# Kernel tuning notes

Hardware: AMD Instinct MI355X
Metric: run time of the kernel (lower is better)

Reference implementation:

```python
import jax, jax.numpy as jnp
import numpy as np

B, S, D, H = 4, 4096, 256, 4
Dh = D // H


def setup_inputs() -> dict:
    key = jax.random.key(0)
    ks = jax.random.split(key, 5)
    scale = 1.0 / np.sqrt(D)
    return {
        "inputs": jax.random.normal(ks[0], (B, S, D), dtype=jnp.float32),
        "Wq": jax.random.normal(ks[1], (D, D), dtype=jnp.float32) * scale,
        "bq": jnp.zeros((D,), jnp.float32),
        "Wk": jax.random.normal(ks[2], (D, D), dtype=jnp.float32) * scale,
        "bk": jnp.zeros((D,), jnp.float32),
        "Wv": jax.random.normal(ks[3], (D, D), dtype=jnp.float32) * scale,
        "bv": jnp.zeros((D,), jnp.float32),
        "Wo": jax.random.normal(ks[4], (D, D), dtype=jnp.float32) * scale,
        "bo": jnp.zeros((D,), jnp.float32),
    }


def reference(inputs, Wq, bq, Wk, bk, Wv, bv, Wo, bo):
    b, s, d = inputs.shape
    # QKV projections
    q = inputs @ Wq + bq
    k = inputs @ Wk + bk
    v = inputs @ Wv + bv
    # separate heads: [B, S, D] -> [B, H, S, Dh]
    def split_heads(x):
        return x.reshape(b, s, H, Dh).transpose(0, 2, 1, 3)
    q, k, v = split_heads(q), split_heads(k), split_heads(v)
    # scaled dot-product attention (no causal mask: mask=False)
    scores = jnp.einsum("bhqd,bhkd->bhqk", q, k) / jnp.sqrt(jnp.float32(Dh))
    weights = jax.nn.softmax(scores, axis=-1)
    attn = jnp.einsum("bhqk,bhkd->bhqd", weights, v)
    # combine heads: [B, H, S, Dh] -> [B, S, D]
    attn = attn.transpose(0, 2, 1, 3).reshape(b, s, d)
    return attn @ Wo + bo
```

## Files before the change

### kernel.cpp

```cpp
#include <hip/hip_runtime.h>
#include <cmath>

#define B_  4
#define S_  4096
#define D_  256
#define H_  4
#define DH_ 64
#define M_TOTAL (B_*S_)
#define QSCALE 0.1803368801111f

typedef __bf16 bf16x8 __attribute__((ext_vector_type(8)));
typedef __bf16 bf16x4 __attribute__((ext_vector_type(4)));
typedef __bf16 bf16x2 __attribute__((ext_vector_type(2)));
typedef float  f32x4  __attribute__((ext_vector_type(4)));
typedef float  f32x16 __attribute__((ext_vector_type(16)));

#define AS1 __attribute__((address_space(1)))
#define AS3 __attribute__((address_space(3)))

__device__ __forceinline__ void g2lds16(const void* g, void* l) {
    __builtin_amdgcn_global_load_lds((AS1 const void*)g, (AS3 void*)l, 16, 0, 0);
}

#if __has_builtin(__builtin_amdgcn_permlane32_swap)
typedef unsigned uint2v __attribute__((ext_vector_type(2)));
__device__ __forceinline__ void plswap(unsigned &a, unsigned &b) {
    uint2v r = __builtin_amdgcn_permlane32_swap(a, b, false, false);
    a = r[0]; b = r[1];
}
#else
__device__ __forceinline__ void plswap(unsigned &a, unsigned &b) {
    unsigned bl = (unsigned)__shfl_xor((int)b, 32);
    unsigned ah = (unsigned)__shfl_xor((int)a, 32);
    bool hi = (threadIdx.x & 32) != 0;
    unsigned na = hi ? bl : a;
    unsigned nb = hi ? b  : ah;
    a = na; b = nb;
}
#endif

__device__ __forceinline__ unsigned pk2(float x, float y) {
    bf16x2 t; t[0] = (__bf16)x; t[1] = (__bf16)y;
    return __builtin_bit_cast(unsigned, t);
}

__global__ __launch_bounds__(256) void prep(const float* __restrict__ X,
                                            const float* __restrict__ W0,
                                            const float* __restrict__ W1,
                                            const float* __restrict__ W2,
                                            const float* __restrict__ W3,
                                            __bf16* __restrict__ Xb,
                                            __bf16* __restrict__ Wt_all) {
    int t = threadIdx.x;
    if (blockIdx.x < 2048) {
        size_t i = ((size_t)blockIdx.x * 256 + t) * 8;
        float4 v0 = *(const float4*)(X + i);
        float4 v1 = *(const float4*)(X + i + 4);
        bf16x8 o;
        o[0] = (__bf16)v0.x; o[1] = (__bf16)v0.y; o[2] = (__bf16)v0.z; o[3] = (__bf16)v0.w;
        o[4] = (__bf16)v1.x; o[5] = (__bf16)v1.y; o[6] = (__bf16)v1.z; o[7] = (__bf16)v1.w;
        *(bf16x8*)(Xb + i) = o;
        return;
    }
    int bid = blockIdx.x - 2048;
    int z = bid >> 6, rem = bid & 63;
    int by = rem >> 3, bx = rem & 7;
    const float* W = (z == 0) ? W0 : (z == 1) ? W1 : (z == 2) ? W2 : W3;
    float wsc = (z == 0) ? QSCALE : 1.0f;
    __bf16* Wt = Wt_all + (size_t)z * 65536;
    __shared__ float tile[32][33];
    int r0 = by * 32, c0 = bx * 32;
#pragma unroll
    for (int e = 0; e < 4; e++) {
        int idx = t + e * 256; int r = idx >> 5, c = idx & 31;
        tile[r][c] = W[(r0 + r) * 256 + c0 + c];
    }
    __syncthreads();
#pragma unroll
    for (int e = 0; e < 4; e++) {
        int idx = t + e * 256; int r = idx >> 5, c = idx & 31;
        Wt[(c0 + r) * 256 + (r0 + c)] = (__bf16)(tile[c][r] * wsc);
    }
}

__global__ __launch_bounds__(256) void gemm_bt(const __bf16* __restrict__ A,
                                               const __bf16* __restrict__ Wt_all,
                                               const float* __restrict__ bias0,
                                               const float* __restrict__ bias1,
                                               const float* __restrict__ bias2,
                                               __bf16* __restrict__ outb,
                                               __bf16* __restrict__ voutb,
                                               float* __restrict__ outf,
                                               int out_is_f32, float bsc0) {
    constexpr int K = 256;
    __shared__ __attribute__((aligned(16))) __bf16 As[128 * 32];
    __shared__ __attribute__((aligned(16))) __bf16 Bs[128 * 32];

    int t = threadIdx.x;
    int lane = t & 63, w = t >> 6;
    int wr = w >> 1, wc = w & 1;
    int l16 = lane & 15, quad = lane >> 4;
    int mbase = blockIdx.x * 128;
    int nbase = blockIdx.y * 128;
    int z = blockIdx.z;
    const __bf16* Bt = Wt_all + (size_t)z * 65536;
    const float* bias = (z == 0) ? bias0 : (z == 1) ? bias1 : bias2;
    float bscale = (z == 0) ? bsc0 : 1.0f;

    f32x4 acc[4][4] = {};

    int srow = t >> 2;
    int sseg = (t & 3) * 8;

    for (int kk = 0; kk < K; kk += 32) {
        __syncthreads();
        g2lds16(A  + (size_t)(mbase +      srow) * K + kk + sseg, (char*)As +        t * 16);
        g2lds16(A  + (size_t)(mbase + 64 + srow) * K + kk + sseg, (char*)As + 4096 + t * 16);
        g2lds16(Bt + (size_t)(nbase +      srow) * K + kk + sseg, (char*)Bs +        t * 16);
        g2lds16(Bt + (size_t)(nbase + 64 + srow) * K + kk + sseg, (char*)Bs + 4096 + t * 16);
        __syncthreads();

        bf16x8 a[4], b[4];
#pragma unroll
        for (int i = 0; i < 4; i++)
            a[i] = *(const bf16x8*)(As + (wr * 64 + i * 16 + l16) * 32 + quad * 8);
#pragma unroll
        for (int j = 0; j < 4; j++)
            b[j] = *(const bf16x8*)(Bs + (wc * 64 + j * 16 + l16) * 32 + quad * 8);
#pragma unroll
        for (int i = 0; i < 4; i++)
#pragma unroll
            for (int j = 0; j < 4; j++)
                acc[i][j] = __builtin_amdgcn_mfma_f32_16x16x32_bf16(a[i], b[j], acc[i][j], 0, 0, 0);
    }

#pragma unroll
    for (int i = 0; i < 4; i++) {
#pragma unroll
        for (int j = 0; j < 4; j++) {
            int col = nbase + wc * 64 + j * 16 + l16;
            float bv = bias[col] * bscale;
            int row0 = mbase + wr * 64 + i * 16 + quad * 4;
            if (out_is_f32) {
#pragma unroll
                for (int r = 0; r < 4; r++)
                    outf[(size_t)(row0 + r) * 256 + col] = acc[i][j][r] + bv;
            } else if (z == 2) {
                int hcol = col >> 6, dh = col & 63;
                int bidx = row0 >> 12, s0 = row0 & 4095;
                bf16x4 pk;
#pragma unroll
                for (int r = 0; r < 4; r++) pk[r] = (__bf16)(acc[i][j][r] + bv);
                *(bf16x4*)(voutb + ((size_t)(bidx * 4 + hcol) * 64 + dh) * 4096 + s0) = pk;
            } else {
#pragma unroll
                for (int r = 0; r < 4; r++)
                    outb[(size_t)z * ((size_t)M_TOTAL * 256) + (size_t)(row0 + r) * 256 + col] =
                        (__bf16)(acc[i][j][r] + bv);
            }
        }
    }
}

__global__ __launch_bounds__(256, 2) void attn(const __bf16* __restrict__ Qb,
                                               const __bf16* __restrict__ Kb,
                                               const __bf16* __restrict__ Vt,
                                               __bf16* __restrict__ Ctx) {
    __shared__ __attribute__((aligned(16))) __bf16 smem[32768];

    int t = threadIdx.x;
    int lane = t & 63, w = t >> 6;
    int l31 = lane & 31, hh = lane >> 5;
    int kw = w & 1, qw2 = w >> 1;

    int lin = blockIdx.x;
    int xcd = lin & 7, j = lin >> 3;
    int bh = xcd * 2 + (j & 1);
    int qblk = j >> 1;
    int b = bh >> 2, hd = bh & 3;
    int qw = qblk * 128 + qw2 * 64;

    const __bf16* Kbase = Kb + (size_t)b * S_ * 256 + hd * 64;
    const __bf16* Vbase = Vt + (size_t)bh * 64 * S_;

    bf16x8 qf[4][2];
#pragma unroll
    for (int ks = 0; ks < 4; ks++)
#pragma unroll
        for (int qt = 0; qt < 2; qt++)
            qf[ks][qt] = *(const bf16x8*)(Qb + (size_t)(b * S_ + qw + qt * 32 + l31) * 256
                                              + hd * 64 + ks * 16 + hh * 8);

    f32x16 acc[2][2] = {};
    float lsum[2] = {0.f, 0.f};

    int srow = t >> 3;
    int sseg = t & 7;

#define STAGE(kv, slot) do {                                                   \
        char* mk = (char*)smem + (slot) * 16384;                               \
        char* mv = mk + 8192;                                                  \
        _Pragma("unroll")                                                      \
        for (int c = 0; c < 2; c++) {                                          \
            int rr = c * 32 + srow;                                            \
            int gseg = (sseg ^ (rr & 7)) * 8;                                  \
            g2lds16(Kbase + (size_t)((kv) + rr) * 256 + gseg,                  \
                    mk + c * 4096 + t * 16);                                   \
            g2lds16(Vbase + (size_t)rr * S_ + (kv) + gseg,                     \
                    mv + c * 4096 + t * 16);                                   \
        }                                                                      \
    } while (0)

    STAGE(0, 0);
    STAGE(64, 1);

    for (int it = 0; it < 64; it++) {
        if (it < 62) {
            STAGE((it + 2) * 64, (it + 2) & 3);
            asm volatile("s_waitcnt vmcnt(8)" ::: "memory");
        } else if (it == 62) {
            asm volatile("s_waitcnt vmcnt(4)" ::: "memory");
        } else {
            asm volatile("s_waitcnt vmcnt(0)" ::: "memory");
        }
        asm volatile("s_barrier" ::: "memory");

        __bf16* Ksp = (__bf16*)((char*)smem + (it & 3) * 16384);
        __bf16* Vsp = Ksp + 4096;

        bf16x8 kf[4];
#pragma unroll
        for (int ks = 0; ks < 4; ks++) {
            int slot = (ks * 2 + hh) ^ (l31 & 7);
            kf[ks] = *(const bf16x8*)(Ksp + (kw * 32 + l31) * 64 + slot * 8);
        }
        f32x16 st[2] = {};
#pragma unroll
        for (int ks = 0; ks < 4; ks++)
#pragma unroll
            for (int qt = 0; qt < 2; qt++)
                st[qt] = __builtin_amdgcn_mfma_f32_32x32x16_bf16(kf[ks], qf[ks][qt], st[qt], 0, 0, 0);

        unsigned dd[2][8];
#pragma unroll
        for (int qt = 0; qt < 2; qt++) {
            float p[16];
#pragma unroll
            for (int r = 0; r < 16; r++) p[r] = __builtin_amdgcn_exp2f(st[qt][r]);
            float s0 = ((p[0] + p[1]) + (p[2] + p[3])) + ((p[4] + p[5]) + (p[6] + p[7]));
            float s1 = ((p[8] + p[9]) + (p[10] + p[11])) + ((p[12] + p[13]) + (p[14] + p[15]));
            lsum[qt] += s0 + s1;
#pragma unroll
            for (int m = 0; m < 4; m++) {
                dd[qt][m * 2]     = pk2(p[4 * m],     p[4 * m + 1]);
                dd[qt][m * 2 + 1] = pk2(p[4 * m + 2], p[4 * m + 3]);
            }
        }

#pragma unroll
        for (int tt = 0; tt < 2; tt++) {
            int tks = kw * 2 + tt;
            bf16x8 pf[2];
#pragma unroll
            for (int qt = 0; qt < 2; qt++) {
                unsigned x0 = dd[qt][4 * tt],     y0 = dd[qt][4 * tt + 2];
                unsigned x1 = dd[qt][4 * tt + 1], y1 = dd[qt][4 * tt + 3];
                plswap(x0, y0);
                plswap(x1, y1);
                union { unsigned u[4]; bf16x8 v; } c;
                c.u[0] = x0; c.u[1] = x1; c.u[2] = y0; c.u[3] = y1;
                pf[qt] = c.v;
            }
#pragma unroll
            for (int mt = 0; mt < 2; mt++) {
                int slot = (tks * 2 + hh) ^ (l31 & 7);
                bf16x8 vf = *(const bf16x8*)(Vsp + (mt * 32 + l31) * 64 + slot * 8);
#pragma unroll
                for (int qt = 0; qt < 2; qt++)
                    acc[mt][qt] = __builtin_amdgcn_mfma_f32_32x32x16_bf16(vf, pf[qt], acc[mt][qt], 0, 0, 0);
            }
        }
    }
#undef STAGE

#pragma unroll
    for (int qt = 0; qt < 2; qt++)
        lsum[qt] += __shfl_xor(lsum[qt], 32);

    __syncthreads();
    float* lsd = (float*)((char*)smem + 32768);
    if (kw == 1) {
#pragma unroll
        for (int mt = 0; mt < 2; mt++)
#pragma unroll
            for (int qt = 0; qt < 2; qt++)
#pragma unroll
                for (int g = 0; g < 4; g++) {
                    f32x4 v;
#pragma unroll
                    for (int e = 0; e < 4; e++) v[e] = acc[mt][qt][4 * g + e];
                    *(f32x4*)((char*)smem + qw2 * 16384
                              + ((mt * 2 + qt) * 4 + g) * 1024 + lane * 16) = v;
                }
        lsd[qw2 * 128 + lane * 2 + 0] = lsum[0];
        lsd[qw2 * 128 + lane * 2 + 1] = lsum[1];
    }
    __syncthreads();
    if (kw == 0) {
        float inv[2];
#pragma unroll
        for (int qt = 0; qt < 2; qt++)
            inv[qt] = 1.f / (lsum[qt] + lsd[qw2 * 128 + lane * 2 + qt]);
#pragma unroll
        for (int mt = 0; mt < 2; mt++)
#pragma unroll
            for (int qt = 0; qt < 2; qt++)
#pragma unroll
                for (int g = 0; g < 4; g++) {
                    f32x4 v = *(const f32x4*)((char*)smem + qw2 * 16384
                                              + ((mt * 2 + qt) * 4 + g) * 1024 + lane * 16);
#pragma unroll
                    for (int e = 0; e < 4; e++) acc[mt][qt][4 * g + e] += v[e];
                }

        __bf16* Es = smem + 18432 + qw2 * 4608;
#pragma unroll
        for (int qt = 0; qt < 2; qt++)
#pragma unroll
            for (int mt = 0; mt < 2; mt++)
#pragma unroll
                for (int rg = 0; rg < 4; rg++) {
                    bf16x4 ov;
#pragma unroll
                    for (int e = 0; e < 4; e++)
                        ov[e] = (__bf16)(acc[mt][qt][4 * rg + e] * inv[qt]);
                    int dhb = mt * 32 + rg * 8 + 4 * hh;
                    *(bf16x4*)(Es + (qt * 32 + l31) * 72 + dhb) = ov;
                }
#pragma unroll
        for (int pass = 0; pass < 8; pass++) {
            int q = pass * 8 + (lane >> 3);
            int col = (lane & 7) * 8;
            bf16x8 val = *(const bf16x8*)(Es + q * 72 + col);
            *(bf16x8*)(Ctx + (size_t)(b * S_ + qw + q) * 256 + hd * 64 + col) = val;
        }
    }
}

extern "C" void kernel_launch(void* const* d_in, const int* in_sizes, int n_in,
                              void* d_out, int out_size, void* d_ws, size_t ws_size,
                              hipStream_t stream) {
    const float* X  = (const float*)d_in[0];
    const float* Wq = (const float*)d_in[1];
    const float* bq = (const float*)d_in[2];
    const float* Wk = (const float*)d_in[3];
    const float* bk = (const float*)d_in[4];
    const float* Wv = (const float*)d_in[5];
    const float* bv = (const float*)d_in[6];
    const float* Wo = (const float*)d_in[7];
    const float* bo = (const float*)d_in[8];
    float* out = (float*)d_out;

    char* ws = (char*)d_ws;
    const size_t MB = 1024 * 1024;
    __bf16* Xb  = (__bf16*)(ws);
    __bf16* Ctx = (__bf16*)(ws);
    __bf16* Wt  = (__bf16*)(ws + 8 * MB);
    __bf16* Qb  = (__bf16*)(ws + 8 * MB + 512 * 1024);
    __bf16* Kb  = (__bf16*)((char*)Qb + 8 * MB);
    __bf16* Vt  = (__bf16*)((char*)Kb + 8 * MB);

    prep<<<dim3(2304), dim3(256), 0, stream>>>(X, Wq, Wk, Wv, Wo, Xb, Wt);
    gemm_bt<<<dim3(M_TOTAL / 128, 2, 3), dim3(256), 0, stream>>>(
        Xb, Wt, bq, bk, bv, Qb, Vt, nullptr, 0, QSCALE);
    attn<<<dim3(512), dim3(256), 0, stream>>>(Qb, Kb, Vt, Ctx);
    gemm_bt<<<dim3(M_TOTAL / 128, 2, 1), dim3(256), 0, stream>>>(
        Ctx, Wt + 3 * 65536, bo, bo, bo, nullptr, nullptr, out, 1, 1.0f);
}
```

Measured before the change: 178.3 us.

## Grow attention blocks to 1024 threads with 4-way KV split and 128-key tiles

The attention kernel now uses 1024-thread blocks covering 256 queries. Each query group is split across four KV-partition waves instead of two, and K/V are staged in 128-key tiles with double buffering in place of four 64-key slots. Each staged tile is shared by more waves and there are half as many loop iterations and barriers. The cost is a deeper sequential cross-wave reduction, with three extra barriers at the end, a wait for all outstanding loads before every iteration, and only 256 blocks, which may leave CUs underused.

```diff
diff --git a/kernel.cpp b/kernel.cpp
--- a/kernel.cpp
+++ b/kernel.cpp
@@ -162,23 +162,23 @@
     }
 }
 
-__global__ __launch_bounds__(256, 2) void attn(const __bf16* __restrict__ Qb,
-                                               const __bf16* __restrict__ Kb,
-                                               const __bf16* __restrict__ Vt,
-                                               __bf16* __restrict__ Ctx) {
+__global__ __launch_bounds__(1024, 4) void attn(const __bf16* __restrict__ Qb,
+                                                const __bf16* __restrict__ Kb,
+                                                const __bf16* __restrict__ Vt,
+                                                __bf16* __restrict__ Ctx) {
     __shared__ __attribute__((aligned(16))) __bf16 smem[32768];
 
     int t = threadIdx.x;
     int lane = t & 63, w = t >> 6;
     int l31 = lane & 31, hh = lane >> 5;
-    int kw = w & 1, qw2 = w >> 1;
+    int kw = w & 3, qw2 = w >> 2;
 
     int lin = blockIdx.x;
     int xcd = lin & 7, j = lin >> 3;
     int bh = xcd * 2 + (j & 1);
     int qblk = j >> 1;
     int b = bh >> 2, hd = bh & 3;
-    int qw = qblk * 128 + qw2 * 64;
+    int qw = qblk * 256 + qw2 * 64;
 
     const __bf16* Kbase = Kb + (size_t)b * S_ * 256 + hd * 64;
     const __bf16* Vbase = Vt + (size_t)bh * 64 * S_;
@@ -194,39 +194,27 @@
     f32x16 acc[2][2] = {};
     float lsum[2] = {0.f, 0.f};
 
-    int srow = t >> 3;
-    int sseg = t & 7;
-
-#define STAGE(kv, slot) do {                                                   \
-        char* mk = (char*)smem + (slot) * 16384;                               \
-        char* mv = mk + 8192;                                                  \
-        _Pragma("unroll")                                                      \
-        for (int c = 0; c < 2; c++) {                                          \
-            int rr = c * 32 + srow;                                            \
-            int gseg = (sseg ^ (rr & 7)) * 8;                                  \
-            g2lds16(Kbase + (size_t)((kv) + rr) * 256 + gseg,                  \
-                    mk + c * 4096 + t * 16);                                   \
-            g2lds16(Vbase + (size_t)rr * S_ + (kv) + gseg,                     \
-                    mv + c * 4096 + t * 16);                                   \
-        }                                                                      \
+    int krow = t >> 3, kseg = t & 7;
+    int vrow = t >> 4, vseg = t & 15;
+    int kgseg = (kseg ^ (krow & 7)) * 8;
+    int vgseg = (vseg ^ (vrow & 7)) * 8;
+
+#define STAGE(kv, sl) do {                                                     \
+        char* mk = (char*)smem + (sl) * 32768;                                 \
+        char* mv = mk + 16384;                                                 \
+        g2lds16(Kbase + (size_t)((kv) + krow) * 256 + kgseg, mk + t * 16);     \
+        g2lds16(Vbase + (size_t)vrow * S_ + (kv) + vgseg,   mv + t * 16);      \
     } while (0)
 
     STAGE(0, 0);
-    STAGE(64, 1);
-
-    for (int it = 0; it < 64; it++) {
-        if (it < 62) {
-            STAGE((it + 2) * 64, (it + 2) & 3);
-            asm volatile("s_waitcnt vmcnt(8)" ::: "memory");
-        } else if (it == 62) {
-            asm volatile("s_waitcnt vmcnt(4)" ::: "memory");
-        } else {
-            asm volatile("s_waitcnt vmcnt(0)" ::: "memory");
-        }
+
+    for (int it = 0; it < 32; it++) {
+        asm volatile("s_waitcnt vmcnt(0)" ::: "memory");
         asm volatile("s_barrier" ::: "memory");
-
-        __bf16* Ksp = (__bf16*)((char*)smem + (it & 3) * 16384);
-        __bf16* Vsp = Ksp + 4096;
+        if (it < 31) STAGE((it + 1) * 128, (it + 1) & 1);
+
+        __bf16* Ksp = (__bf16*)((char*)smem + (it & 1) * 32768);
+        __bf16* Vsp = Ksp + 8192;
 
         bf16x8 kf[4];
 #pragma unroll
@@ -274,7 +262,7 @@
 #pragma unroll
             for (int mt = 0; mt < 2; mt++) {
                 int slot = (tks * 2 + hh) ^ (l31 & 7);
-                bf16x8 vf = *(const bf16x8*)(Vsp + (mt * 32 + l31) * 64 + slot * 8);
+                bf16x8 vf = *(const bf16x8*)(Vsp + (mt * 32 + l31) * 128 + slot * 8);
 #pragma unroll
                 for (int qt = 0; qt < 2; qt++)
                     acc[mt][qt] = __builtin_amdgcn_mfma_f32_32x32x16_bf16(vf, pf[qt], acc[mt][qt], 0, 0, 0);
@@ -288,42 +276,56 @@
         lsum[qt] += __shfl_xor(lsum[qt], 32);
 
     __syncthreads();
-    float* lsd = (float*)((char*)smem + 32768);
-    if (kw == 1) {
-#pragma unroll
-        for (int mt = 0; mt < 2; mt++)
-#pragma unroll
-            for (int qt = 0; qt < 2; qt++)
-#pragma unroll
-                for (int g = 0; g < 4; g++) {
-                    f32x4 v;
-#pragma unroll
-                    for (int e = 0; e < 4; e++) v[e] = acc[mt][qt][4 * g + e];
-                    *(f32x4*)((char*)smem + qw2 * 16384
-                              + ((mt * 2 + qt) * 4 + g) * 1024 + lane * 16) = v;
-                }
-        lsd[qw2 * 128 + lane * 2 + 0] = lsum[0];
-        lsd[qw2 * 128 + lane * 2 + 1] = lsum[1];
-    }
-    __syncthreads();
+    float* lsd = (float*)smem;
+    lsd[w * 128 + lane * 2 + 0] = lsum[0];
+    lsd[w * 128 + lane * 2 + 1] = lsum[1];
+    __syncthreads();
+    float inv[2] = {0.f, 0.f};
     if (kw == 0) {
-        float inv[2];
-#pragma unroll
-        for (int qt = 0; qt < 2; qt++)
-            inv[qt] = 1.f / (lsum[qt] + lsd[qw2 * 128 + lane * 2 + qt]);
-#pragma unroll
-        for (int mt = 0; mt < 2; mt++)
-#pragma unroll
-            for (int qt = 0; qt < 2; qt++)
-#pragma unroll
-                for (int g = 0; g < 4; g++) {
-                    f32x4 v = *(const f32x4*)((char*)smem + qw2 * 16384
-                                              + ((mt * 2 + qt) * 4 + g) * 1024 + lane * 16);
-#pragma unroll
-                    for (int e = 0; e < 4; e++) acc[mt][qt][4 * g + e] += v[e];
-                }
-
-        __bf16* Es = smem + 18432 + qw2 * 4608;
+#pragma unroll
+        for (int qt = 0; qt < 2; qt++) {
+            float s = 0.f;
+#pragma unroll
+            for (int kk = 0; kk < 4; kk++)
+                s += lsd[(qw2 * 4 + kk) * 128 + lane * 2 + qt];
+            inv[qt] = 1.f / s;
+        }
+    }
+    __syncthreads();
+
+#define DUMPACC() do {                                                         \
+        _Pragma("unroll") for (int mt = 0; mt < 2; mt++)                       \
+        _Pragma("unroll") for (int qt = 0; qt < 2; qt++)                       \
+        _Pragma("unroll") for (int g = 0; g < 4; g++) {                        \
+            f32x4 v;                                                           \
+            _Pragma("unroll") for (int e = 0; e < 4; e++)                      \
+                v[e] = acc[mt][qt][4 * g + e];                                 \
+            *(f32x4*)((char*)smem + qw2 * 16384                                \
+                      + ((mt * 2 + qt) * 4 + g) * 1024 + lane * 16) = v;       \
+        }                                                                      \
+    } while (0)
+#define ADDACC() do {                                                          \
+        _Pragma("unroll") for (int mt = 0; mt < 2; mt++)                       \
+        _Pragma("unroll") for (int qt = 0; qt < 2; qt++)                       \
+        _Pragma("unroll") for (int g = 0; g < 4; g++) {                        \
+            f32x4 v = *(const f32x4*)((char*)smem + qw2 * 16384                \
+                      + ((mt * 2 + qt) * 4 + g) * 1024 + lane * 16);           \
+            _Pragma("unroll") for (int e = 0; e < 4; e++)                      \
+                acc[mt][qt][4 * g + e] += v[e];                                \
+        }                                                                      \
+    } while (0)
+
+    if (kw == 3) DUMPACC();
+    __syncthreads();
+    if (kw == 2) { ADDACC(); DUMPACC(); }
+    __syncthreads();
+    if (kw == 1) { ADDACC(); DUMPACC(); }
+    __syncthreads();
+    if (kw == 0) {
+        ADDACC();
+        asm volatile("" ::: "memory");
+
+        __bf16* Es = (__bf16*)((char*)smem + qw2 * 16384);
 #pragma unroll
         for (int qt = 0; qt < 2; qt++)
 #pragma unroll
@@ -345,6 +347,8 @@
             *(bf16x8*)(Ctx + (size_t)(b * S_ + qw + q) * 256 + hd * 64 + col) = val;
         }
     }
+#undef DUMPACC
+#undef ADDACC
 }
 
 extern "C" void kernel_launch(void* const* d_in, const int* in_sizes, int n_in,
@@ -373,7 +377,7 @@
     prep<<<dim3(2304), dim3(256), 0, stream>>>(X, Wq, Wk, Wv, Wo, Xb, Wt);
     gemm_bt<<<dim3(M_TOTAL / 128, 2, 3), dim3(256), 0, stream>>>(
         Xb, Wt, bq, bk, bv, Qb, Vt, nullptr, 0, QSCALE);
-    attn<<<dim3(512), dim3(256), 0, stream>>>(Qb, Kb, Vt, Ctx);
+    attn<<<dim3(256), dim3(1024), 0, stream>>>(Qb, Kb, Vt, Ctx);
     gemm_bt<<<dim3(M_TOTAL / 128, 2, 1), dim3(256), 0, stream>>>(
         Ctx, Wt + 3 * 65536, bo, bo, bo, nullptr, nullptr, out, 1, 1.0f);
 }
```

New measurement: 294.0 us. +64.9%, slower.

## Software-pipeline QK^T of next tile with softmax and PV of current tile

Applied to the files above, without the earlier changes.

Restructures the attention inner loop so the QK^T MFMAs for tile it+1 are issued before the exp/pack/PV work for tile it. The loop is unrolled by two and ping-pongs between two score register sets. The K/V prefetch now runs three tiles ahead using all four LDS slots, with matching vmcnt waits. The aim is to overlap MFMA work with the exp2 and permlane VALU work and to hide global-load latency better. The cost is 32 more VGPRs for the second score buffer, which may pressure occupancy or cause spills.

```diff
diff --git a/kernel.cpp b/kernel.cpp
--- a/kernel.cpp
+++ b/kernel.cpp
@@ -211,76 +211,93 @@
         }                                                                      \
     } while (0)
 
+#define QKSTEP(TILE, SN) do {                                                  \
+        __bf16* Ksp = (__bf16*)((char*)smem + ((TILE) & 3) * 16384);           \
+        bf16x8 kfv[4];                                                         \
+        _Pragma("unroll")                                                      \
+        for (int ks = 0; ks < 4; ks++) {                                       \
+            int slot = (ks * 2 + hh) ^ (l31 & 7);                              \
+            kfv[ks] = *(const bf16x8*)(Ksp + (kw * 32 + l31) * 64 + slot * 8); \
+        }                                                                      \
+        _Pragma("unroll")                                                      \
+        for (int qt = 0; qt < 2; qt++) SN[qt] = (f32x16){};                    \
+        _Pragma("unroll")                                                      \
+        for (int ks = 0; ks < 4; ks++)                                         \
+            _Pragma("unroll")                                                  \
+            for (int qt = 0; qt < 2; qt++)                                     \
+                SN[qt] = __builtin_amdgcn_mfma_f32_32x32x16_bf16(              \
+                    kfv[ks], qf[ks][qt], SN[qt], 0, 0, 0);                     \
+    } while (0)
+
+#define SMPV(IT, SC) do {                                                      \
+        __bf16* Vsp = (__bf16*)((char*)smem + ((IT) & 3) * 16384) + 4096;      \
+        unsigned dd[2][8];                                                     \
+        _Pragma("unroll")                                                      \
+        for (int qt = 0; qt < 2; qt++) {                                       \
+            float p[16];                                                       \
+            _Pragma("unroll")                                                  \
+            for (int r = 0; r < 16; r++)                                       \
+                p[r] = __builtin_amdgcn_exp2f(SC[qt][r]);                      \
+            float s0 = ((p[0]+p[1])+(p[2]+p[3]))+((p[4]+p[5])+(p[6]+p[7]));    \
+            float s1 = ((p[8]+p[9])+(p[10]+p[11]))+((p[12]+p[13])+(p[14]+p[15])); \
+            lsum[qt] += s0 + s1;                                               \
+            _Pragma("unroll")                                                  \
+            for (int m = 0; m < 4; m++) {                                      \
+                dd[qt][m*2]   = pk2(p[4*m],   p[4*m+1]);                       \
+                dd[qt][m*2+1] = pk2(p[4*m+2], p[4*m+3]);                       \
+            }                                                                  \
+        }                                                                      \
+        _Pragma("unroll")                                                      \
+        for (int tt = 0; tt < 2; tt++) {                                       \
+            int tks = kw * 2 + tt;                                             \
+            bf16x8 pf[2];                                                      \
+            _Pragma("unroll")                                                  \
+            for (int qt = 0; qt < 2; qt++) {                                   \
+                unsigned x0 = dd[qt][4*tt],   y0 = dd[qt][4*tt+2];             \
+                unsigned x1 = dd[qt][4*tt+1], y1 = dd[qt][4*tt+3];             \
+                plswap(x0, y0);                                                \
+                plswap(x1, y1);                                                \
+                union { unsigned u[4]; bf16x8 v; } c;                          \
+                c.u[0] = x0; c.u[1] = x1; c.u[2] = y0; c.u[3] = y1;            \
+                pf[qt] = c.v;                                                  \
+            }                                                                  \
+            _Pragma("unroll")                                                  \
+            for (int mt = 0; mt < 2; mt++) {                                   \
+                int slot = (tks * 2 + hh) ^ (l31 & 7);                         \
+                bf16x8 vf = *(const bf16x8*)(Vsp + (mt*32 + l31)*64 + slot*8); \
+                _Pragma("unroll")                                              \
+                for (int qt = 0; qt < 2; qt++)                                 \
+                    acc[mt][qt] = __builtin_amdgcn_mfma_f32_32x32x16_bf16(     \
+                        vf, pf[qt], acc[mt][qt], 0, 0, 0);                     \
+            }                                                                  \
+        }                                                                      \
+    } while (0)
+
+#define BODY(IT, SC, SN) do {                                                  \
+        if ((IT) < 62) asm volatile("s_waitcnt vmcnt(4)" ::: "memory");        \
+        else           asm volatile("s_waitcnt vmcnt(0)" ::: "memory");        \
+        asm volatile("s_barrier" ::: "memory");                                \
+        if ((IT) <= 60) STAGE(((IT) + 3) * 64, ((IT) + 3) & 3);                \
+        if ((IT) < 63) QKSTEP((IT) + 1, SN);                                   \
+        SMPV(IT, SC);                                                          \
+    } while (0)
+
+    f32x16 stA[2], stB[2];
+
     STAGE(0, 0);
     STAGE(64, 1);
-
-    for (int it = 0; it < 64; it++) {
-        if (it < 62) {
-            STAGE((it + 2) * 64, (it + 2) & 3);
-            asm volatile("s_waitcnt vmcnt(8)" ::: "memory");
-        } else if (it == 62) {
-            asm volatile("s_waitcnt vmcnt(4)" ::: "memory");
-        } else {
-            asm volatile("s_waitcnt vmcnt(0)" ::: "memory");
-        }
-        asm volatile("s_barrier" ::: "memory");
-
-        __bf16* Ksp = (__bf16*)((char*)smem + (it & 3) * 16384);
-        __bf16* Vsp = Ksp + 4096;
-
-        bf16x8 kf[4];
-#pragma unroll
-        for (int ks = 0; ks < 4; ks++) {
-            int slot = (ks * 2 + hh) ^ (l31 & 7);
-            kf[ks] = *(const bf16x8*)(Ksp + (kw * 32 + l31) * 64 + slot * 8);
-        }
-        f32x16 st[2] = {};
-#pragma unroll
-        for (int ks = 0; ks < 4; ks++)
-#pragma unroll
-            for (int qt = 0; qt < 2; qt++)
-                st[qt] = __builtin_amdgcn_mfma_f32_32x32x16_bf16(kf[ks], qf[ks][qt], st[qt], 0, 0, 0);
-
-        unsigned dd[2][8];
-#pragma unroll
-        for (int qt = 0; qt < 2; qt++) {
-            float p[16];
-#pragma unroll
-            for (int r = 0; r < 16; r++) p[r] = __builtin_amdgcn_exp2f(st[qt][r]);
-            float s0 = ((p[0] + p[1]) + (p[2] + p[3])) + ((p[4] + p[5]) + (p[6] + p[7]));
-            float s1 = ((p[8] + p[9]) + (p[10] + p[11])) + ((p[12] + p[13]) + (p[14] + p[15]));
-            lsum[qt] += s0 + s1;
-#pragma unroll
-            for (int m = 0; m < 4; m++) {
-                dd[qt][m * 2]     = pk2(p[4 * m],     p[4 * m + 1]);
-                dd[qt][m * 2 + 1] = pk2(p[4 * m + 2], p[4 * m + 3]);
-            }
-        }
-
-#pragma unroll
-        for (int tt = 0; tt < 2; tt++) {
-            int tks = kw * 2 + tt;
-            bf16x8 pf[2];
-#pragma unroll
-            for (int qt = 0; qt < 2; qt++) {
-                unsigned x0 = dd[qt][4 * tt],     y0 = dd[qt][4 * tt + 2];
-                unsigned x1 = dd[qt][4 * tt + 1], y1 = dd[qt][4 * tt + 3];
-                plswap(x0, y0);
-                plswap(x1, y1);
-                union { unsigned u[4]; bf16x8 v; } c;
-                c.u[0] = x0; c.u[1] = x1; c.u[2] = y0; c.u[3] = y1;
-                pf[qt] = c.v;
-            }
-#pragma unroll
-            for (int mt = 0; mt < 2; mt++) {
-                int slot = (tks * 2 + hh) ^ (l31 & 7);
-                bf16x8 vf = *(const bf16x8*)(Vsp + (mt * 32 + l31) * 64 + slot * 8);
-#pragma unroll
-                for (int qt = 0; qt < 2; qt++)
-                    acc[mt][qt] = __builtin_amdgcn_mfma_f32_32x32x16_bf16(vf, pf[qt], acc[mt][qt], 0, 0, 0);
-            }
-        }
-    }
+    STAGE(128, 2);
+    asm volatile("s_waitcnt vmcnt(8)" ::: "memory");
+    asm volatile("s_barrier" ::: "memory");
+    QKSTEP(0, stA);
+
+    for (int it = 0; it < 64; it += 2) {
+        BODY(it,     stA, stB);
+        BODY(it + 1, stB, stA);
+    }
+#undef BODY
+#undef SMPV
+#undef QKSTEP
 #undef STAGE
 
 #pragma unroll
```

Result: no change. 177.2 us (-0.6%).
